# Performance work log

Measured on AMD Instinct MI355X. Metric: run time of the kernel, lower is better.

Reference implementation:

```python
import jax, jax.numpy as jnp
import numpy as np

SLOPE = 25.0  # fast_sigmoid surrogate slope
T, B, N_IN, H, A = 128, 4096, 64, 32, 4
ACT_OUT = 100 * A

@jax.custom_vjp
def spike(x):
    return (x > 0).astype(x.dtype)

def _spk_fwd(x):
    return (x > 0).astype(x.dtype), x

def _spk_bwd(x, g):
    # fast_sigmoid surrogate: d/dx = 1 / (slope*|x| + 1)^2
    return (g / (SLOPE * jnp.abs(x) + 1.0) ** 2,)

spike.defvjp(_spk_fwd, _spk_bwd)

def lif(cur, mem, beta, thr):
    # snntorch Leaky, reset_mechanism='subtract': reset uses previous-step membrane
    reset = spike(mem - thr)
    mem = beta * mem + cur - reset * thr
    return spike(mem - thr), mem

def _linear_init(key, out_d, in_d):
    kw, kb = jax.random.split(key)
    lim = 1.0 / np.sqrt(in_d)
    W = jax.random.uniform(kw, (out_d, in_d), jnp.float32, -lim, lim)
    b = jax.random.uniform(kb, (out_d,), jnp.float32, -lim, lim)
    return W, b

def setup_inputs() -> dict:
    key = jax.random.key(0)
    ks = jax.random.split(key, 12)
    inputs = jax.random.normal(ks[0], (T, B, N_IN), jnp.float32)
    W_in, b_in = _linear_init(ks[1], N_IN, N_IN)
    W1, b1 = _linear_init(ks[2], H, N_IN)
    W2, b2 = _linear_init(ks[3], H, H)
    W3, b3 = _linear_init(ks[4], H, H)
    W4, b4 = _linear_init(ks[5], H, H)
    W5, b5 = _linear_init(ks[6], H, H)
    W6, b6 = _linear_init(ks[7], H, H)
    W7, b7 = _linear_init(ks[8], H, H)
    W_actor, b_actor = _linear_init(ks[9], ACT_OUT, H)
    W_critic, b_critic = _linear_init(ks[10], 1, H)
    beta_critic = jnp.float32(0.95)  # learn_beta=True
    am = np.zeros((ACT_OUT, A), np.float32)
    for row in range(A):
        am[row * 100:(row + 1) * 100, row] = 0.01
    action_mat = jnp.asarray(am)
    return dict(inputs=inputs, W_in=W_in, b_in=b_in, W1=W1, b1=b1, W2=W2, b2=b2,
                W3=W3, b3=b3, W4=W4, b4=b4, W5=W5, b5=b5, W6=W6, b6=b6,
                W7=W7, b7=b7, W_actor=W_actor, b_actor=b_actor,
                W_critic=W_critic, b_critic=b_critic,
                beta_critic=beta_critic, action_mat=action_mat)

def reference(inputs, W_in, b_in, W1, b1, W2, b2, W3, b3, W4, b4, W5, b5,
              W6, b6, W7, b7, W_actor, b_actor, W_critic, b_critic,
              beta_critic, action_mat):
    Bn = inputs.shape[1]
    z = lambda d: jnp.zeros((Bn, d), inputs.dtype)
    carry0 = (z(N_IN), z(H), z(H), z(H), z(H), z(H), z(H), z(H), z(1), z(ACT_OUT))
    layers = ((W1, b1, 0.65, 0.25), (W2, b2, 0.85, 1.0), (W3, b3, 0.85, 1.0),
              (W4, b4, 0.95, 1.0), (W5, b5, 0.95, 1.0), (W6, b6, 0.95, 1.0),
              (W7, b7, 0.95, 1.0))
    def step(carry, x_t):
        m_in, m1, m2, m3, m4, m5, m6, m7, mc, ma = carry
        s, m_in = lif(x_t @ W_in.T + b_in, m_in, 0.65, 0.25)
        mems = [m1, m2, m3, m4, m5, m6, m7]
        new_mems = []
        for (W, b, beta, thr), m in zip(layers, mems):
            s, m = lif(s @ W.T + b, m, beta, thr)
            new_mems.append(m)
        spk_a, ma = lif(s @ W_actor.T + b_actor, ma, 0.95, 1.0)
        _, mc = lif(s @ W_critic.T + b_critic, mc, beta_critic, 100.0)
        val = mc
        actions = spk_a @ action_mat
        return (m_in, *new_mems, mc, ma), (val, actions)
    _, (vals, actions) = jax.lax.scan(step, carry0, inputs)
    return vals, actions  # [T,B,1], [T,B,A]
```

## Files before the change

### kernel.cpp

```cpp
#include <hip/hip_runtime.h>

#define TSTEPS 128
#define BATCH  4096
#define WPB    16

#define OFF_WTIN 0
#define OFF_WT1  4096
#define OFF_WTH  6144
#define OFF_WTA  12288
#define OFF_WC   25088
#define OFF_TAB  25120
#define OFF_XBUF 25224
#define LDS_FLOATS (OFF_XBUF + WPB * 64)
#define LDS_BYTES  (LDS_FLOATS * 4)

#define LIF(M, CUR, BETA, THR) {                                           \
    float r_ = ((M) > (THR)) ? (THR) : 0.0f;                               \
    (M) = __fsub_rn(__fadd_rn(__fmul_rn((BETA), (M)), (CUR)), r_); }

#define HDOT32(MASK, COLP, OUTV) {                                         \
    float acc_ = 0.0f; unsigned mm_ = (MASK);                              \
    while (mm_) {                                                          \
      int j_ = __builtin_ctz(mm_); mm_ &= mm_ - 1;                         \
      acc_ = __fadd_rn(acc_, (COLP)[j_ * 32]);                             \
    }                                                                      \
    OUTV = acc_; }

extern "C" __global__ __launch_bounds__(1024, 1)
void snn_actor_critic(const float* __restrict__ inputs,
                      const float* __restrict__ Win, const float* __restrict__ bin_,
                      const float* __restrict__ W1,  const float* __restrict__ b1,
                      const float* __restrict__ W2,  const float* __restrict__ b2,
                      const float* __restrict__ W3,  const float* __restrict__ b3,
                      const float* __restrict__ W4,  const float* __restrict__ b4,
                      const float* __restrict__ W5,  const float* __restrict__ b5,
                      const float* __restrict__ W6,  const float* __restrict__ b6,
                      const float* __restrict__ W7,  const float* __restrict__ b7,
                      const float* __restrict__ Wa,  const float* __restrict__ ba,
                      const float* __restrict__ Wc,  const float* __restrict__ bc,
                      const float* __restrict__ betac, const float* __restrict__ am,
                      float* __restrict__ out)
{
  extern __shared__ float lds[];
  const int tid  = threadIdx.x;
  const int lane = tid & 63;
  const int l32  = lane & 31;

  #pragma unroll
  for (int it = 0; it < 4; ++it) {
    int idx = tid + it * 1024; int i = idx >> 6, j = idx & 63;
    lds[OFF_WTIN + j * 64 + i] = Win[idx];
  }
  #pragma unroll
  for (int it = 0; it < 2; ++it) {
    int idx = tid + it * 1024; int i = idx >> 6, j = idx & 63;
    lds[OFF_WT1 + j * 32 + i] = W1[idx];
  }
  {
    int i = tid >> 5, j = tid & 31; int d = j * 32 + i;
    lds[OFF_WTH + 0 * 1024 + d] = W2[tid];
    lds[OFF_WTH + 1 * 1024 + d] = W3[tid];
    lds[OFF_WTH + 2 * 1024 + d] = W4[tid];
    lds[OFF_WTH + 3 * 1024 + d] = W5[tid];
    lds[OFF_WTH + 4 * 1024 + d] = W6[tid];
    lds[OFF_WTH + 5 * 1024 + d] = W7[tid];
  }
  for (int idx = tid; idx < 12800; idx += 1024) {
    int k = idx >> 5, j = idx & 31;
    lds[OFF_WTA + j * 400 + k] = Wa[idx];
  }
  if (tid < 32) lds[OFF_WC + tid] = Wc[tid];
  if (tid == 0) {
    float a = 0.0f; lds[OFF_TAB] = 0.0f; float step = am[0];
    for (int n = 1; n <= 100; ++n) { a = __fadd_rn(a, step); lds[OFF_TAB + n] = a; }
  }

  float bin_f = bin_[lane];
  float bh0 = b1[l32], bh1 = b2[l32], bh2 = b3[l32], bh3 = b4[l32],
        bh4 = b5[l32], bh5 = b6[l32], bh6 = b7[l32];
  float ba0 = ba[lane],       ba1 = ba[lane + 64],  ba2 = ba[lane + 128],
        ba3 = ba[lane + 192], ba4 = ba[lane + 256], ba5 = ba[lane + 320],
        ba6 = (lane < 16) ? ba[lane + 384] : 0.0f;
  float bc_f    = bc[0];
  float beta_cf = betac[0];

  __syncthreads();

  const int  wave = tid >> 6;
  const long b    = (long)blockIdx.x * WPB + wave;
  float* xw = lds + OFF_XBUF + wave * 64;
  const float* wcol = lds + OFF_WTIN + lane;
  const float* col1 = lds + OFF_WT1  + l32;
  const float* colh = lds + OFF_WTH  + l32;
  const float* wab  = lds + OFF_WTA  + lane;
  const float* wcp  = lds + OFF_WC;
  const float* tab  = lds + OFF_TAB;
  const float* inp  = inputs + b * 64 + lane;
  float* vout = out + b;
  float* aout = out + (long)TSTEPS * BATCH + b * 4 + lane;

  float m_in = 0.0f;
  float mh0 = 0.0f, mh1 = 0.0f, mh2 = 0.0f, mh3 = 0.0f, mh4 = 0.0f, mh5 = 0.0f, mh6 = 0.0f;
  float ma0 = 0.0f, ma1 = 0.0f, ma2 = 0.0f, ma3 = 0.0f, ma4 = 0.0f, ma5 = 0.0f, ma6 = 0.0f;
  float mc  = 0.0f;

  for (int t = 0; t < TSTEPS; ++t) {
    xw[lane] = inp[(long)t * (BATCH * 64)];

    float acc = 0.0f;
    #pragma unroll
    for (int j = 0; j < 64; ++j)
      acc = __builtin_fmaf(xw[j], wcol[j * 64], acc);
    float cur = __fadd_rn(acc, bin_f);
    LIF(m_in, cur, 0.65f, 0.25f);
    unsigned long long s64 = __ballot(__fsub_rn(m_in, 0.25f) > 0.0f);

    float d1 = 0.0f;
    { unsigned long long mm_ = s64;
      while (mm_) {
        int j_ = (int)__builtin_ctzll(mm_); mm_ &= mm_ - 1;
        d1 = __fadd_rn(d1, col1[j_ * 32]);
      } }
    float cur1 = __fadd_rn(d1, bh0);
    LIF(mh0, cur1, 0.65f, 0.25f);
    unsigned k1 = (unsigned)__ballot(__fsub_rn(mh0, 0.25f) > 0.0f);

    float d2; HDOT32(k1, colh + 0 * 1024, d2);
    float cur2 = __fadd_rn(d2, bh1);
    LIF(mh1, cur2, 0.85f, 1.0f);
    unsigned k2 = (unsigned)__ballot(__fsub_rn(mh1, 1.0f) > 0.0f);

    float d3; HDOT32(k2, colh + 1 * 1024, d3);
    float cur3 = __fadd_rn(d3, bh2);
    LIF(mh2, cur3, 0.85f, 1.0f);
    unsigned k3 = (unsigned)__ballot(__fsub_rn(mh2, 1.0f) > 0.0f);

    float d4; HDOT32(k3, colh + 2 * 1024, d4);
    float cur4 = __fadd_rn(d4, bh3);
    LIF(mh3, cur4, 0.95f, 1.0f);
    unsigned k4 = (unsigned)__ballot(__fsub_rn(mh3, 1.0f) > 0.0f);

    float d5; HDOT32(k4, colh + 3 * 1024, d5);
    float cur5 = __fadd_rn(d5, bh4);
    LIF(mh4, cur5, 0.95f, 1.0f);
    unsigned k5 = (unsigned)__ballot(__fsub_rn(mh4, 1.0f) > 0.0f);

    float d6; HDOT32(k5, colh + 4 * 1024, d6);
    float cur6 = __fadd_rn(d6, bh5);
    LIF(mh5, cur6, 0.95f, 1.0f);
    unsigned k6 = (unsigned)__ballot(__fsub_rn(mh5, 1.0f) > 0.0f);

    float d7; HDOT32(k6, colh + 5 * 1024, d7);
    float cur7 = __fadd_rn(d7, bh6);
    LIF(mh6, cur7, 0.95f, 1.0f);
    unsigned k7 = (unsigned)__ballot(__fsub_rn(mh6, 1.0f) > 0.0f);

    float ca0 = 0.0f, ca1 = 0.0f, ca2 = 0.0f, ca3 = 0.0f, ca4 = 0.0f, ca5 = 0.0f, ca6 = 0.0f;
    { unsigned mm_ = k7;
      while (mm_) {
        int j_ = __builtin_ctz(mm_); mm_ &= mm_ - 1;
        const float* rp = wab + j_ * 400;
        ca0 = __fadd_rn(ca0, rp[0]);   ca1 = __fadd_rn(ca1, rp[64]);
        ca2 = __fadd_rn(ca2, rp[128]); ca3 = __fadd_rn(ca3, rp[192]);
        ca4 = __fadd_rn(ca4, rp[256]); ca5 = __fadd_rn(ca5, rp[320]);
        ca6 = __fadd_rn(ca6, rp[384]);
      } }
    float cua0 = __fadd_rn(ca0, ba0), cua1 = __fadd_rn(ca1, ba1),
          cua2 = __fadd_rn(ca2, ba2), cua3 = __fadd_rn(ca3, ba3),
          cua4 = __fadd_rn(ca4, ba4), cua5 = __fadd_rn(ca5, ba5),
          cua6 = __fadd_rn(ca6, ba6);
    unsigned long long sa0, sa1, sa2, sa3, sa4, sa5, sa6;
    LIF(ma0, cua0, 0.95f, 1.0f); sa0 = __ballot(__fsub_rn(ma0, 1.0f) > 0.0f);
    LIF(ma1, cua1, 0.95f, 1.0f); sa1 = __ballot(__fsub_rn(ma1, 1.0f) > 0.0f);
    LIF(ma2, cua2, 0.95f, 1.0f); sa2 = __ballot(__fsub_rn(ma2, 1.0f) > 0.0f);
    LIF(ma3, cua3, 0.95f, 1.0f); sa3 = __ballot(__fsub_rn(ma3, 1.0f) > 0.0f);
    LIF(ma4, cua4, 0.95f, 1.0f); sa4 = __ballot(__fsub_rn(ma4, 1.0f) > 0.0f);
    LIF(ma5, cua5, 0.95f, 1.0f); sa5 = __ballot(__fsub_rn(ma5, 1.0f) > 0.0f);
    LIF(ma6, cua6, 0.95f, 1.0f); sa6 = __ballot(__fsub_rn(ma6, 1.0f) > 0.0f);

    int c0 = __popcll(sa0) + __popcll(sa1 & 0xFFFFFFFFFULL);
    int c1 = __popcll(sa1 >> 36) + __popcll(sa2) + __popcll(sa3 & 0xFFULL);
    int c2 = __popcll(sa3 >> 8) + __popcll(sa4 & 0xFFFFFFFFFFFULL);
    int c3 = __popcll(sa4 >> 44) + __popcll(sa5) + __popcll(sa6 & 0xFFFFULL);

    float cc = 0.0f;
    { unsigned mm_ = k7;
      while (mm_) { int j_ = __builtin_ctz(mm_); mm_ &= mm_ - 1;
                    cc = __fadd_rn(cc, wcp[j_]); } }
    float curc = __fadd_rn(cc, bc_f);
    LIF(mc, curc, beta_cf, 100.0f);

    if (lane == 0) vout[(long)t * BATCH] = mc;
    if (lane < 4) {
      int cnt = (lane == 0) ? c0 : (lane == 1) ? c1 : (lane == 2) ? c2 : c3;
      aout[(long)t * BATCH * 4] = tab[cnt];
    }
  }
}

extern "C" void kernel_launch(void* const* d_in, const int* in_sizes, int n_in,
                              void* d_out, int out_size, void* d_ws, size_t ws_size,
                              hipStream_t stream) {
  (void)in_sizes; (void)n_in; (void)out_size; (void)d_ws; (void)ws_size;
  hipFuncSetAttribute((const void*)snn_actor_critic,
                      hipFuncAttributeMaxDynamicSharedMemorySize, LDS_BYTES);
  const float* I    = (const float*)d_in[0];
  const float* Win  = (const float*)d_in[1];  const float* bin_ = (const float*)d_in[2];
  const float* W1   = (const float*)d_in[3];  const float* b1   = (const float*)d_in[4];
  const float* W2   = (const float*)d_in[5];  const float* b2   = (const float*)d_in[6];
  const float* W3   = (const float*)d_in[7];  const float* b3   = (const float*)d_in[8];
  const float* W4   = (const float*)d_in[9];  const float* b4   = (const float*)d_in[10];
  const float* W5   = (const float*)d_in[11]; const float* b5   = (const float*)d_in[12];
  const float* W6   = (const float*)d_in[13]; const float* b6   = (const float*)d_in[14];
  const float* W7   = (const float*)d_in[15]; const float* b7   = (const float*)d_in[16];
  const float* Wa   = (const float*)d_in[17]; const float* ba   = (const float*)d_in[18];
  const float* Wc   = (const float*)d_in[19]; const float* bc   = (const float*)d_in[20];
  const float* betc = (const float*)d_in[21]; const float* am   = (const float*)d_in[22];
  float* out = (float*)d_out;

  snn_actor_critic<<<dim3(BATCH / WPB), dim3(1024), LDS_BYTES, stream>>>(
      I, Win, bin_, W1, b1, W2, b2, W3, b3, W4, b4, W5, b5, W6, b6, W7, b7,
      Wa, ba, Wc, bc, betc, am, out);
}
```

Before: 643.7 us.

## Replace sparse spike-mask loops with dense unrolled FMA dot products and prefetch input

Replaces the data-dependent ctz/while loops over spike bitmasks with fully unrolled dense loops that multiply each weight by a 0/1 spike value via FMA. This removes the serial scalar loop control and branch divergence, and lets the LDS loads be issued ahead of time. The cost is doing every multiply-add even when spikes are sparse, which means more LDS traffic. It also software-prefetches the next timestep's input into a register so the global load latency overlaps with the current step's compute.

```diff
diff --git a/kernel.cpp b/kernel.cpp
--- a/kernel.cpp
+++ b/kernel.cpp
@@ -18,11 +18,12 @@
     float r_ = ((M) > (THR)) ? (THR) : 0.0f;                               \
     (M) = __fsub_rn(__fadd_rn(__fmul_rn((BETA), (M)), (CUR)), r_); }
 
-#define HDOT32(MASK, COLP, OUTV) {                                         \
-    float acc_ = 0.0f; unsigned mm_ = (MASK);                              \
-    while (mm_) {                                                          \
-      int j_ = __builtin_ctz(mm_); mm_ &= mm_ - 1;                         \
-      acc_ = __fadd_rn(acc_, (COLP)[j_ * 32]);                             \
+#define DDOT32(MASK, COLP, OUTV) {                                         \
+    float acc_ = 0.0f;                                                     \
+    _Pragma("unroll")                                                      \
+    for (int j_ = 0; j_ < 32; ++j_) {                                      \
+      float sj_ = (((MASK) >> j_) & 1u) ? 1.0f : 0.0f;                     \
+      acc_ = __builtin_fmaf(sj_, (COLP)[j_ * 32], acc_);                   \
     }                                                                      \
     OUTV = acc_; }
 
@@ -104,8 +105,12 @@
   float ma0 = 0.0f, ma1 = 0.0f, ma2 = 0.0f, ma3 = 0.0f, ma4 = 0.0f, ma5 = 0.0f, ma6 = 0.0f;
   float mc  = 0.0f;
 
+  float xnext = inp[0];
+
   for (int t = 0; t < TSTEPS; ++t) {
-    xw[lane] = inp[(long)t * (BATCH * 64)];
+    xw[lane] = xnext;
+    if (t + 1 < TSTEPS)
+      xnext = inp[(long)(t + 1) * (BATCH * 64)];
 
     float acc = 0.0f;
     #pragma unroll
@@ -116,55 +121,58 @@
     unsigned long long s64 = __ballot(__fsub_rn(m_in, 0.25f) > 0.0f);
 
     float d1 = 0.0f;
-    { unsigned long long mm_ = s64;
-      while (mm_) {
-        int j_ = (int)__builtin_ctzll(mm_); mm_ &= mm_ - 1;
-        d1 = __fadd_rn(d1, col1[j_ * 32]);
-      } }
+    #pragma unroll
+    for (int j = 0; j < 64; ++j) {
+      float sj = ((s64 >> j) & 1ULL) ? 1.0f : 0.0f;
+      d1 = __builtin_fmaf(sj, col1[j * 32], d1);
+    }
     float cur1 = __fadd_rn(d1, bh0);
     LIF(mh0, cur1, 0.65f, 0.25f);
     unsigned k1 = (unsigned)__ballot(__fsub_rn(mh0, 0.25f) > 0.0f);
 
-    float d2; HDOT32(k1, colh + 0 * 1024, d2);
+    float d2; DDOT32(k1, colh + 0 * 1024, d2);
     float cur2 = __fadd_rn(d2, bh1);
     LIF(mh1, cur2, 0.85f, 1.0f);
     unsigned k2 = (unsigned)__ballot(__fsub_rn(mh1, 1.0f) > 0.0f);
 
-    float d3; HDOT32(k2, colh + 1 * 1024, d3);
+    float d3; DDOT32(k2, colh + 1 * 1024, d3);
     float cur3 = __fadd_rn(d3, bh2);
     LIF(mh2, cur3, 0.85f, 1.0f);
     unsigned k3 = (unsigned)__ballot(__fsub_rn(mh2, 1.0f) > 0.0f);
 
-    float d4; HDOT32(k3, colh + 2 * 1024, d4);
+    float d4; DDOT32(k3, colh + 2 * 1024, d4);
     float cur4 = __fadd_rn(d4, bh3);
     LIF(mh3, cur4, 0.95f, 1.0f);
     unsigned k4 = (unsigned)__ballot(__fsub_rn(mh3, 1.0f) > 0.0f);
 
-    float d5; HDOT32(k4, colh + 3 * 1024, d5);
+    float d5; DDOT32(k4, colh + 3 * 1024, d5);
     float cur5 = __fadd_rn(d5, bh4);
     LIF(mh4, cur5, 0.95f, 1.0f);
     unsigned k5 = (unsigned)__ballot(__fsub_rn(mh4, 1.0f) > 0.0f);
 
-    float d6; HDOT32(k5, colh + 4 * 1024, d6);
+    float d6; DDOT32(k5, colh + 4 * 1024, d6);
     float cur6 = __fadd_rn(d6, bh5);
     LIF(mh5, cur6, 0.95f, 1.0f);
     unsigned k6 = (unsigned)__ballot(__fsub_rn(mh5, 1.0f) > 0.0f);
 
-    float d7; HDOT32(k6, colh + 5 * 1024, d7);
+    float d7; DDOT32(k6, colh + 5 * 1024, d7);
     float cur7 = __fadd_rn(d7, bh6);
     LIF(mh6, cur7, 0.95f, 1.0f);
     unsigned k7 = (unsigned)__ballot(__fsub_rn(mh6, 1.0f) > 0.0f);
 
     float ca0 = 0.0f, ca1 = 0.0f, ca2 = 0.0f, ca3 = 0.0f, ca4 = 0.0f, ca5 = 0.0f, ca6 = 0.0f;
-    { unsigned mm_ = k7;
-      while (mm_) {
-        int j_ = __builtin_ctz(mm_); mm_ &= mm_ - 1;
-        const float* rp = wab + j_ * 400;
-        ca0 = __fadd_rn(ca0, rp[0]);   ca1 = __fadd_rn(ca1, rp[64]);
-        ca2 = __fadd_rn(ca2, rp[128]); ca3 = __fadd_rn(ca3, rp[192]);
-        ca4 = __fadd_rn(ca4, rp[256]); ca5 = __fadd_rn(ca5, rp[320]);
-        ca6 = __fadd_rn(ca6, rp[384]);
-      } }
+    #pragma unroll
+    for (int j = 0; j < 32; ++j) {
+      float sj = ((k7 >> j) & 1u) ? 1.0f : 0.0f;
+      const float* rp = wab + j * 400;
+      ca0 = __builtin_fmaf(sj, rp[0],   ca0);
+      ca1 = __builtin_fmaf(sj, rp[64],  ca1);
+      ca2 = __builtin_fmaf(sj, rp[128], ca2);
+      ca3 = __builtin_fmaf(sj, rp[192], ca3);
+      ca4 = __builtin_fmaf(sj, rp[256], ca4);
+      ca5 = __builtin_fmaf(sj, rp[320], ca5);
+      ca6 = __builtin_fmaf(sj, rp[384], ca6);
+    }
     float cua0 = __fadd_rn(ca0, ba0), cua1 = __fadd_rn(ca1, ba1),
           cua2 = __fadd_rn(ca2, ba2), cua3 = __fadd_rn(ca3, ba3),
           cua4 = __fadd_rn(ca4, ba4), cua5 = __fadd_rn(ca5, ba5),
@@ -184,9 +192,11 @@
     int c3 = __popcll(sa4 >> 44) + __popcll(sa5) + __popcll(sa6 & 0xFFFFULL);
 
     float cc = 0.0f;
-    { unsigned mm_ = k7;
-      while (mm_) { int j_ = __builtin_ctz(mm_); mm_ &= mm_ - 1;
-                    cc = __fadd_rn(cc, wcp[j_]); } }
+    #pragma unroll
+    for (int j = 0; j < 32; ++j) {
+      float sj = ((k7 >> j) & 1u) ? 1.0f : 0.0f;
+      cc = __builtin_fmaf(sj, wcp[j], cc);
+    }
     float curc = __fadd_rn(cc, bc_f);
     LIF(mc, curc, beta_cf, 100.0f);
 
```

Result: slower. 1.537 ms (+138.8%).

## Process two batch elements per wave with packed FP32 FMAs and dense spike matmuls

Applied to the files above, without the earlier changes.

Each wave now handles two batch elements at once, keeping paired membrane states in float2 and using v_pk_fma_f32 inline asm to evaluate both samples per instruction. The sparse ctz-loop accumulation over spike masks is replaced by fully unrolled dense FMAs, where SGPR-held 0/1 selector pairs multiply interleaved weight pairs. Weights are relaid into float2-interleaved LDS, blocks shrink to 8 waves, and the next timestep's input is prefetched. This removes divergent scalar loops and halves per-sample instruction overhead, but dense FMA changes summation order relative to the sparse adds, which may shift spike thresholds, and it does work even when spikes are sparse.

```diff
diff --git a/kernel.cpp b/kernel.cpp
--- a/kernel.cpp
+++ b/kernel.cpp
@@ -2,31 +2,69 @@
 
 #define TSTEPS 128
 #define BATCH  4096
-#define WPB    16
-
-#define OFF_WTIN 0
-#define OFF_WT1  4096
-#define OFF_WTH  6144
-#define OFF_WTA  12288
-#define OFF_WC   25088
-#define OFF_TAB  25120
-#define OFF_XBUF 25224
-#define LDS_FLOATS (OFF_XBUF + WPB * 64)
+#define WPB    8
+
+typedef float f32x2 __attribute__((ext_vector_type(2)));
+typedef unsigned long long u64;
+
+#define O2_WIN 0
+#define O2_W1  2048
+#define O2_WH  3072
+#define O2_WA  6144
+#define O2_WC  13312
+#define O2_X   13328
+#define TABF   27680
+#define LDS_FLOATS (TABF + 104)
 #define LDS_BYTES  (LDS_FLOATS * 4)
 
-#define LIF(M, CUR, BETA, THR) {                                           \
-    float r_ = ((M) > (THR)) ? (THR) : 0.0f;                               \
-    (M) = __fsub_rn(__fadd_rn(__fmul_rn((BETA), (M)), (CUR)), r_); }
-
-#define HDOT32(MASK, COLP, OUTV) {                                         \
-    float acc_ = 0.0f; unsigned mm_ = (MASK);                              \
-    while (mm_) {                                                          \
-      int j_ = __builtin_ctz(mm_); mm_ &= mm_ - 1;                         \
-      acc_ = __fadd_rn(acc_, (COLP)[j_ * 32]);                             \
-    }                                                                      \
-    OUTV = acc_; }
-
-extern "C" __global__ __launch_bounds__(1024, 1)
+#define C00 0ull
+#define C10 0x3f800000ull
+#define C01 (0x3f800000ull << 32)
+#define C11 (0x3f800000ull | (0x3f800000ull << 32))
+
+#define SEL2(M0, M1, J)                                                    \
+  ((((M0) >> (J)) & 1u) ? ((((M1) >> (J)) & 1u) ? C11 : C10)               \
+                        : ((((M1) >> (J)) & 1u) ? C01 : C00))
+
+#define PKFMA_SLO(ACC, SEL, W2)                                            \
+  asm("v_pk_fma_f32 %0, %1, %2, %0 op_sel:[0,0,0] op_sel_hi:[1,0,1]"       \
+      : "+v"(ACC) : "s"(SEL), "v"(W2))
+#define PKFMA_SHI(ACC, SEL, W2)                                            \
+  asm("v_pk_fma_f32 %0, %1, %2, %0 op_sel:[0,1,0] op_sel_hi:[1,1,1]"       \
+      : "+v"(ACC) : "s"(SEL), "v"(W2))
+#define PKFMA_VLO(ACC, XY, W2)                                             \
+  asm("v_pk_fma_f32 %0, %1, %2, %0 op_sel:[0,0,0] op_sel_hi:[1,0,1]"       \
+      : "+v"(ACC) : "v"(XY), "v"(W2))
+#define PKFMA_VHI(ACC, XY, W2)                                             \
+  asm("v_pk_fma_f32 %0, %1, %2, %0 op_sel:[0,1,0] op_sel_hi:[1,1,1]"       \
+      : "+v"(ACC) : "v"(XY), "v"(W2))
+
+#define LIF2(M, CX, CY, BETA, THR) {                                       \
+    float rx_ = (M[0] > (THR)) ? (THR) : 0.0f;                             \
+    float ry_ = (M[1] > (THR)) ? (THR) : 0.0f;                             \
+    M[0] = __fsub_rn(__fadd_rn(__fmul_rn((BETA), M[0]), (CX)), rx_);       \
+    M[1] = __fsub_rn(__fadd_rn(__fmul_rn((BETA), M[1]), (CY)), ry_); }
+
+#define SPIKES32(M, ACC, BIAS, BETA, THR, M0, M1) {                        \
+    float cx_ = __fadd_rn(ACC[0], (BIAS));                                 \
+    float cy_ = __fadd_rn(ACC[1], (BIAS));                                 \
+    LIF2(M, cx_, cy_, BETA, THR);                                          \
+    u64 b0_ = __ballot(__fsub_rn(M[0], (THR)) > 0.0f);                     \
+    u64 b1_ = __ballot(__fsub_rn(M[1], (THR)) > 0.0f);                     \
+    M0 = __builtin_amdgcn_readfirstlane((unsigned)b0_);                    \
+    M1 = __builtin_amdgcn_readfirstlane((unsigned)b1_); }
+
+#define DENSE32_PK(ACC, BASE2, M0, M1) {                                   \
+    _Pragma("unroll")                                                      \
+    for (int jp_ = 0; jp_ < 16; ++jp_) {                                   \
+      f32x2 w2_ = (BASE2)[jp_ * 32 + i32];                                 \
+      u64 sA_ = SEL2(M0, M1, 2 * jp_);                                     \
+      u64 sB_ = SEL2(M0, M1, 2 * jp_ + 1);                                 \
+      PKFMA_SLO(ACC, sA_, w2_);                                            \
+      PKFMA_SHI(ACC, sB_, w2_);                                            \
+    } }
+
+extern "C" __global__ __launch_bounds__(512, 1)
 void snn_actor_critic(const float* __restrict__ inputs,
                       const float* __restrict__ Win, const float* __restrict__ bin_,
                       const float* __restrict__ W1,  const float* __restrict__ b1,
@@ -42,158 +80,198 @@
                       float* __restrict__ out)
 {
   extern __shared__ float lds[];
+  f32x2* lds2 = (f32x2*)lds;
   const int tid  = threadIdx.x;
   const int lane = tid & 63;
-  const int l32  = lane & 31;
+  const int i32  = lane & 31;
 
   #pragma unroll
   for (int it = 0; it < 4; ++it) {
-    int idx = tid + it * 1024; int i = idx >> 6, j = idx & 63;
-    lds[OFF_WTIN + j * 64 + i] = Win[idx];
+    int e = tid + it * 512; int jp = e >> 6, l = e & 63;
+    lds2[O2_WIN + e] = (f32x2){Win[l * 64 + 2 * jp], Win[l * 64 + 2 * jp + 1]};
   }
   #pragma unroll
   for (int it = 0; it < 2; ++it) {
-    int idx = tid + it * 1024; int i = idx >> 6, j = idx & 63;
-    lds[OFF_WT1 + j * 32 + i] = W1[idx];
+    int e = tid + it * 512; int jp = e >> 5, i = e & 31;
+    lds2[O2_W1 + e] = (f32x2){W1[i * 64 + 2 * jp], W1[i * 64 + 2 * jp + 1]};
   }
   {
-    int i = tid >> 5, j = tid & 31; int d = j * 32 + i;
-    lds[OFF_WTH + 0 * 1024 + d] = W2[tid];
-    lds[OFF_WTH + 1 * 1024 + d] = W3[tid];
-    lds[OFF_WTH + 2 * 1024 + d] = W4[tid];
-    lds[OFF_WTH + 3 * 1024 + d] = W5[tid];
-    lds[OFF_WTH + 4 * 1024 + d] = W6[tid];
-    lds[OFF_WTH + 5 * 1024 + d] = W7[tid];
-  }
-  for (int idx = tid; idx < 12800; idx += 1024) {
-    int k = idx >> 5, j = idx & 31;
-    lds[OFF_WTA + j * 400 + k] = Wa[idx];
-  }
-  if (tid < 32) lds[OFF_WC + tid] = Wc[tid];
+    int jp = tid >> 5, i = tid & 31;
+    lds2[O2_WH + 0 * 512 + tid] = (f32x2){W2[i * 32 + 2 * jp], W2[i * 32 + 2 * jp + 1]};
+    lds2[O2_WH + 1 * 512 + tid] = (f32x2){W3[i * 32 + 2 * jp], W3[i * 32 + 2 * jp + 1]};
+    lds2[O2_WH + 2 * 512 + tid] = (f32x2){W4[i * 32 + 2 * jp], W4[i * 32 + 2 * jp + 1]};
+    lds2[O2_WH + 3 * 512 + tid] = (f32x2){W5[i * 32 + 2 * jp], W5[i * 32 + 2 * jp + 1]};
+    lds2[O2_WH + 4 * 512 + tid] = (f32x2){W6[i * 32 + 2 * jp], W6[i * 32 + 2 * jp + 1]};
+    lds2[O2_WH + 5 * 512 + tid] = (f32x2){W7[i * 32 + 2 * jp], W7[i * 32 + 2 * jp + 1]};
+  }
+  for (int e = tid; e < 7168; e += 512) {
+    int r = e >> 10, rem = e & 1023, jp = rem >> 6, l = rem & 63;
+    int k = r * 64 + l;
+    lds2[O2_WA + e] = (k < 400)
+        ? (f32x2){Wa[k * 32 + 2 * jp], Wa[k * 32 + 2 * jp + 1]}
+        : (f32x2){0.0f, 0.0f};
+  }
+  if (tid < 16) lds2[O2_WC + tid] = (f32x2){Wc[2 * tid], Wc[2 * tid + 1]};
   if (tid == 0) {
-    float a = 0.0f; lds[OFF_TAB] = 0.0f; float step = am[0];
-    for (int n = 1; n <= 100; ++n) { a = __fadd_rn(a, step); lds[OFF_TAB + n] = a; }
+    float a = 0.0f; lds[TABF] = 0.0f; float step = am[0];
+    for (int n = 1; n <= 100; ++n) { a = __fadd_rn(a, step); lds[TABF + n] = a; }
   }
 
   float bin_f = bin_[lane];
-  float bh0 = b1[l32], bh1 = b2[l32], bh2 = b3[l32], bh3 = b4[l32],
-        bh4 = b5[l32], bh5 = b6[l32], bh6 = b7[l32];
-  float ba0 = ba[lane],       ba1 = ba[lane + 64],  ba2 = ba[lane + 128],
-        ba3 = ba[lane + 192], ba4 = ba[lane + 256], ba5 = ba[lane + 320],
-        ba6 = (lane < 16) ? ba[lane + 384] : 0.0f;
-  float bc_f    = bc[0];
+  float bh0 = b1[i32], bh1 = b2[i32], bh2 = b3[i32], bh3 = b4[i32],
+        bh4 = b5[i32], bh5 = b6[i32], bh6 = b7[i32];
+  float bA0 = ba[lane],       bA1 = ba[lane + 64],  bA2 = ba[lane + 128],
+        bA3 = ba[lane + 192], bA4 = ba[lane + 256], bA5 = ba[lane + 320],
+        bA6 = (lane < 16) ? ba[lane + 384] : 0.0f;
+  float bc_f = bc[0];
   float beta_cf = betac[0];
 
   __syncthreads();
 
   const int  wave = tid >> 6;
-  const long b    = (long)blockIdx.x * WPB + wave;
-  float* xw = lds + OFF_XBUF + wave * 64;
-  const float* wcol = lds + OFF_WTIN + lane;
-  const float* col1 = lds + OFF_WT1  + l32;
-  const float* colh = lds + OFF_WTH  + l32;
-  const float* wab  = lds + OFF_WTA  + lane;
-  const float* wcp  = lds + OFF_WC;
-  const float* tab  = lds + OFF_TAB;
-  const float* inp  = inputs + b * 64 + lane;
-  float* vout = out + b;
-  float* aout = out + (long)TSTEPS * BATCH + b * 4 + lane;
-
-  float m_in = 0.0f;
-  float mh0 = 0.0f, mh1 = 0.0f, mh2 = 0.0f, mh3 = 0.0f, mh4 = 0.0f, mh5 = 0.0f, mh6 = 0.0f;
-  float ma0 = 0.0f, ma1 = 0.0f, ma2 = 0.0f, ma3 = 0.0f, ma4 = 0.0f, ma5 = 0.0f, ma6 = 0.0f;
-  float mc  = 0.0f;
+  const long gw   = (long)blockIdx.x * WPB + wave;
+  const long e0   = gw * 2;
+  const f32x2* winb = lds2 + O2_WIN;
+  const f32x2* w1b  = lds2 + O2_W1;
+  const f32x2* whb  = lds2 + O2_WH;
+  const f32x2* wab  = lds2 + O2_WA;
+  const f32x2* wcb  = lds2 + O2_WC;
+  const f32x2* xw2  = lds2 + O2_X + wave * 64;
+  f32x2* xw2w = lds2 + O2_X + wave * 64;
+  const float* tab  = lds + TABF;
+  const float* inp0 = inputs + e0 * 64 + lane;
+  const float* inp1 = inputs + (e0 + 1) * 64 + lane;
+  float* vout = out + e0;
+  float* aout = out + (long)TSTEPS * BATCH + e0 * 4;
+
+  f32x2 mI = {0,0};
+  f32x2 m1 = {0,0}, m2 = {0,0}, m3 = {0,0}, m4 = {0,0}, m5 = {0,0}, m6 = {0,0}, m7 = {0,0};
+  f32x2 A0 = {0,0}, A1 = {0,0}, A2 = {0,0}, A3 = {0,0}, A4 = {0,0}, A5 = {0,0}, A6 = {0,0};
+  f32x2 mc = {0,0};
+
+  float xn0 = inp0[0], xn1 = inp1[0];
 
   for (int t = 0; t < TSTEPS; ++t) {
-    xw[lane] = inp[(long)t * (BATCH * 64)];
-
-    float acc = 0.0f;
+    xw2w[lane] = (f32x2){xn0, xn1};
+    if (t + 1 < TSTEPS) {
+      xn0 = inp0[(long)(t + 1) * (BATCH * 64)];
+      xn1 = inp1[(long)(t + 1) * (BATCH * 64)];
+    }
+
+    f32x2 aI = {0,0};
     #pragma unroll
-    for (int j = 0; j < 64; ++j)
-      acc = __builtin_fmaf(xw[j], wcol[j * 64], acc);
-    float cur = __fadd_rn(acc, bin_f);
-    LIF(m_in, cur, 0.65f, 0.25f);
-    unsigned long long s64 = __ballot(__fsub_rn(m_in, 0.25f) > 0.0f);
-
-    float d1 = 0.0f;
-    { unsigned long long mm_ = s64;
-      while (mm_) {
-        int j_ = (int)__builtin_ctzll(mm_); mm_ &= mm_ - 1;
-        d1 = __fadd_rn(d1, col1[j_ * 32]);
-      } }
-    float cur1 = __fadd_rn(d1, bh0);
-    LIF(mh0, cur1, 0.65f, 0.25f);
-    unsigned k1 = (unsigned)__ballot(__fsub_rn(mh0, 0.25f) > 0.0f);
-
-    float d2; HDOT32(k1, colh + 0 * 1024, d2);
-    float cur2 = __fadd_rn(d2, bh1);
-    LIF(mh1, cur2, 0.85f, 1.0f);
-    unsigned k2 = (unsigned)__ballot(__fsub_rn(mh1, 1.0f) > 0.0f);
-
-    float d3; HDOT32(k2, colh + 1 * 1024, d3);
-    float cur3 = __fadd_rn(d3, bh2);
-    LIF(mh2, cur3, 0.85f, 1.0f);
-    unsigned k3 = (unsigned)__ballot(__fsub_rn(mh2, 1.0f) > 0.0f);
-
-    float d4; HDOT32(k3, colh + 2 * 1024, d4);
-    float cur4 = __fadd_rn(d4, bh3);
-    LIF(mh3, cur4, 0.95f, 1.0f);
-    unsigned k4 = (unsigned)__ballot(__fsub_rn(mh3, 1.0f) > 0.0f);
-
-    float d5; HDOT32(k4, colh + 3 * 1024, d5);
-    float cur5 = __fadd_rn(d5, bh4);
-    LIF(mh4, cur5, 0.95f, 1.0f);
-    unsigned k5 = (unsigned)__ballot(__fsub_rn(mh4, 1.0f) > 0.0f);
-
-    float d6; HDOT32(k5, colh + 4 * 1024, d6);
-    float cur6 = __fadd_rn(d6, bh5);
-    LIF(mh5, cur6, 0.95f, 1.0f);
-    unsigned k6 = (unsigned)__ballot(__fsub_rn(mh5, 1.0f) > 0.0f);
-
-    float d7; HDOT32(k6, colh + 5 * 1024, d7);
-    float cur7 = __fadd_rn(d7, bh6);
-    LIF(mh6, cur7, 0.95f, 1.0f);
-    unsigned k7 = (unsigned)__ballot(__fsub_rn(mh6, 1.0f) > 0.0f);
-
-    float ca0 = 0.0f, ca1 = 0.0f, ca2 = 0.0f, ca3 = 0.0f, ca4 = 0.0f, ca5 = 0.0f, ca6 = 0.0f;
-    { unsigned mm_ = k7;
-      while (mm_) {
-        int j_ = __builtin_ctz(mm_); mm_ &= mm_ - 1;
-        const float* rp = wab + j_ * 400;
-        ca0 = __fadd_rn(ca0, rp[0]);   ca1 = __fadd_rn(ca1, rp[64]);
-        ca2 = __fadd_rn(ca2, rp[128]); ca3 = __fadd_rn(ca3, rp[192]);
-        ca4 = __fadd_rn(ca4, rp[256]); ca5 = __fadd_rn(ca5, rp[320]);
-        ca6 = __fadd_rn(ca6, rp[384]);
-      } }
-    float cua0 = __fadd_rn(ca0, ba0), cua1 = __fadd_rn(ca1, ba1),
-          cua2 = __fadd_rn(ca2, ba2), cua3 = __fadd_rn(ca3, ba3),
-          cua4 = __fadd_rn(ca4, ba4), cua5 = __fadd_rn(ca5, ba5),
-          cua6 = __fadd_rn(ca6, ba6);
-    unsigned long long sa0, sa1, sa2, sa3, sa4, sa5, sa6;
-    LIF(ma0, cua0, 0.95f, 1.0f); sa0 = __ballot(__fsub_rn(ma0, 1.0f) > 0.0f);
-    LIF(ma1, cua1, 0.95f, 1.0f); sa1 = __ballot(__fsub_rn(ma1, 1.0f) > 0.0f);
-    LIF(ma2, cua2, 0.95f, 1.0f); sa2 = __ballot(__fsub_rn(ma2, 1.0f) > 0.0f);
-    LIF(ma3, cua3, 0.95f, 1.0f); sa3 = __ballot(__fsub_rn(ma3, 1.0f) > 0.0f);
-    LIF(ma4, cua4, 0.95f, 1.0f); sa4 = __ballot(__fsub_rn(ma4, 1.0f) > 0.0f);
-    LIF(ma5, cua5, 0.95f, 1.0f); sa5 = __ballot(__fsub_rn(ma5, 1.0f) > 0.0f);
-    LIF(ma6, cua6, 0.95f, 1.0f); sa6 = __ballot(__fsub_rn(ma6, 1.0f) > 0.0f);
-
-    int c0 = __popcll(sa0) + __popcll(sa1 & 0xFFFFFFFFFULL);
-    int c1 = __popcll(sa1 >> 36) + __popcll(sa2) + __popcll(sa3 & 0xFFULL);
-    int c2 = __popcll(sa3 >> 8) + __popcll(sa4 & 0xFFFFFFFFFFFULL);
-    int c3 = __popcll(sa4 >> 44) + __popcll(sa5) + __popcll(sa6 & 0xFFFFULL);
-
-    float cc = 0.0f;
-    { unsigned mm_ = k7;
-      while (mm_) { int j_ = __builtin_ctz(mm_); mm_ &= mm_ - 1;
-                    cc = __fadd_rn(cc, wcp[j_]); } }
-    float curc = __fadd_rn(cc, bc_f);
-    LIF(mc, curc, beta_cf, 100.0f);
-
-    if (lane == 0) vout[(long)t * BATCH] = mc;
-    if (lane < 4) {
-      int cnt = (lane == 0) ? c0 : (lane == 1) ? c1 : (lane == 2) ? c2 : c3;
-      aout[(long)t * BATCH * 4] = tab[cnt];
+    for (int jp = 0; jp < 32; ++jp) {
+      f32x2 w2 = winb[jp * 64 + lane];
+      f32x2 xa = xw2[2 * jp];
+      f32x2 xb = xw2[2 * jp + 1];
+      PKFMA_VLO(aI, xa, w2);
+      PKFMA_VHI(aI, xb, w2);
+    }
+    {
+      float cx = __fadd_rn(aI[0], bin_f), cy = __fadd_rn(aI[1], bin_f);
+      LIF2(mI, cx, cy, 0.65f, 0.25f);
+    }
+    u64 ib0 = __ballot(__fsub_rn(mI[0], 0.25f) > 0.0f);
+    u64 ib1 = __ballot(__fsub_rn(mI[1], 0.25f) > 0.0f);
+    unsigned s0lo = __builtin_amdgcn_readfirstlane((unsigned)ib0);
+    unsigned s0hi = __builtin_amdgcn_readfirstlane((unsigned)(ib0 >> 32));
+    unsigned s1lo = __builtin_amdgcn_readfirstlane((unsigned)ib1);
+    unsigned s1hi = __builtin_amdgcn_readfirstlane((unsigned)(ib1 >> 32));
+
+    f32x2 a1 = {0,0};
+    DENSE32_PK(a1, w1b, s0lo, s1lo);
+    DENSE32_PK(a1, w1b + 16 * 32, s0hi, s1hi);
+    unsigned k1a, k1b; SPIKES32(m1, a1, bh0, 0.65f, 0.25f, k1a, k1b);
+
+    f32x2 a2 = {0,0}; DENSE32_PK(a2, whb + 0 * 512, k1a, k1b);
+    unsigned k2a, k2b; SPIKES32(m2, a2, bh1, 0.85f, 1.0f, k2a, k2b);
+    f32x2 a3 = {0,0}; DENSE32_PK(a3, whb + 1 * 512, k2a, k2b);
+    unsigned k3a, k3b; SPIKES32(m3, a3, bh2, 0.85f, 1.0f, k3a, k3b);
+    f32x2 a4 = {0,0}; DENSE32_PK(a4, whb + 2 * 512, k3a, k3b);
+    unsigned k4a, k4b; SPIKES32(m4, a4, bh3, 0.95f, 1.0f, k4a, k4b);
+    f32x2 a5 = {0,0}; DENSE32_PK(a5, whb + 3 * 512, k4a, k4b);
+    unsigned k5a, k5b; SPIKES32(m5, a5, bh4, 0.95f, 1.0f, k5a, k5b);
+    f32x2 a6 = {0,0}; DENSE32_PK(a6, whb + 4 * 512, k5a, k5b);
+    unsigned k6a, k6b; SPIKES32(m6, a6, bh5, 0.95f, 1.0f, k6a, k6b);
+    f32x2 a7 = {0,0}; DENSE32_PK(a7, whb + 5 * 512, k6a, k6b);
+    unsigned k7a, k7b; SPIKES32(m7, a7, bh6, 0.95f, 1.0f, k7a, k7b);
+
+    f32x2 c0 = {0,0}, c1 = {0,0}, c2 = {0,0}, c3 = {0,0},
+          c4 = {0,0}, c5 = {0,0}, c6 = {0,0}, cc = {0,0};
+    #pragma unroll
+    for (int jp = 0; jp < 16; ++jp) {
+      u64 sA = SEL2(k7a, k7b, 2 * jp);
+      u64 sB = SEL2(k7a, k7b, 2 * jp + 1);
+      f32x2 w0 = wab[0 * 1024 + jp * 64 + lane];
+      f32x2 w1v = wab[1 * 1024 + jp * 64 + lane];
+      f32x2 w2v = wab[2 * 1024 + jp * 64 + lane];
+      f32x2 w3v = wab[3 * 1024 + jp * 64 + lane];
+      f32x2 w4v = wab[4 * 1024 + jp * 64 + lane];
+      f32x2 w5v = wab[5 * 1024 + jp * 64 + lane];
+      f32x2 w6v = wab[6 * 1024 + jp * 64 + lane];
+      f32x2 wcv = wcb[jp];
+      PKFMA_SLO(c0, sA, w0);  PKFMA_SHI(c0, sB, w0);
+      PKFMA_SLO(c1, sA, w1v); PKFMA_SHI(c1, sB, w1v);
+      PKFMA_SLO(c2, sA, w2v); PKFMA_SHI(c2, sB, w2v);
+      PKFMA_SLO(c3, sA, w3v); PKFMA_SHI(c3, sB, w3v);
+      PKFMA_SLO(c4, sA, w4v); PKFMA_SHI(c4, sB, w4v);
+      PKFMA_SLO(c5, sA, w5v); PKFMA_SHI(c5, sB, w5v);
+      PKFMA_SLO(c6, sA, w6v); PKFMA_SHI(c6, sB, w6v);
+      PKFMA_SLO(cc, sA, wcv); PKFMA_SHI(cc, sB, wcv);
+    }
+    u64 sa0, sa1, sa2, sa3, sa4, sa5, sa6;
+    u64 ta0, ta1, ta2, ta3, ta4, ta5, ta6;
+    {
+      float cx, cy;
+      cx = __fadd_rn(c0[0], bA0); cy = __fadd_rn(c0[1], bA0);
+      LIF2(A0, cx, cy, 0.95f, 1.0f);
+      sa0 = __ballot(__fsub_rn(A0[0], 1.0f) > 0.0f);
+      ta0 = __ballot(__fsub_rn(A0[1], 1.0f) > 0.0f);
+      cx = __fadd_rn(c1[0], bA1); cy = __fadd_rn(c1[1], bA1);
+      LIF2(A1, cx, cy, 0.95f, 1.0f);
+      sa1 = __ballot(__fsub_rn(A1[0], 1.0f) > 0.0f);
+      ta1 = __ballot(__fsub_rn(A1[1], 1.0f) > 0.0f);
+      cx = __fadd_rn(c2[0], bA2); cy = __fadd_rn(c2[1], bA2);
+      LIF2(A2, cx, cy, 0.95f, 1.0f);
+      sa2 = __ballot(__fsub_rn(A2[0], 1.0f) > 0.0f);
+      ta2 = __ballot(__fsub_rn(A2[1], 1.0f) > 0.0f);
+      cx = __fadd_rn(c3[0], bA3); cy = __fadd_rn(c3[1], bA3);
+      LIF2(A3, cx, cy, 0.95f, 1.0f);
+      sa3 = __ballot(__fsub_rn(A3[0], 1.0f) > 0.0f);
+      ta3 = __ballot(__fsub_rn(A3[1], 1.0f) > 0.0f);
+      cx = __fadd_rn(c4[0], bA4); cy = __fadd_rn(c4[1], bA4);
+      LIF2(A4, cx, cy, 0.95f, 1.0f);
+      sa4 = __ballot(__fsub_rn(A4[0], 1.0f) > 0.0f);
+      ta4 = __ballot(__fsub_rn(A4[1], 1.0f) > 0.0f);
+      cx = __fadd_rn(c5[0], bA5); cy = __fadd_rn(c5[1], bA5);
+      LIF2(A5, cx, cy, 0.95f, 1.0f);
+      sa5 = __ballot(__fsub_rn(A5[0], 1.0f) > 0.0f);
+      ta5 = __ballot(__fsub_rn(A5[1], 1.0f) > 0.0f);
+      cx = __fadd_rn(c6[0], bA6); cy = __fadd_rn(c6[1], bA6);
+      LIF2(A6, cx, cy, 0.95f, 1.0f);
+      sa6 = __ballot(__fsub_rn(A6[0], 1.0f) > 0.0f);
+      ta6 = __ballot(__fsub_rn(A6[1], 1.0f) > 0.0f);
+    }
+    int g0 = __popcll(sa0) + __popcll(sa1 & 0xFFFFFFFFFULL);
+    int g1 = __popcll(sa1 >> 36) + __popcll(sa2) + __popcll(sa3 & 0xFFULL);
+    int g2 = __popcll(sa3 >> 8) + __popcll(sa4 & 0xFFFFFFFFFFFULL);
+    int g3 = __popcll(sa4 >> 44) + __popcll(sa5) + __popcll(sa6 & 0xFFFFULL);
+    int h0 = __popcll(ta0) + __popcll(ta1 & 0xFFFFFFFFFULL);
+    int h1 = __popcll(ta1 >> 36) + __popcll(ta2) + __popcll(ta3 & 0xFFULL);
+    int h2 = __popcll(ta3 >> 8) + __popcll(ta4 & 0xFFFFFFFFFFFULL);
+    int h3 = __popcll(ta4 >> 44) + __popcll(ta5) + __popcll(ta6 & 0xFFFFULL);
+
+    {
+      float cx = __fadd_rn(cc[0], bc_f), cy = __fadd_rn(cc[1], bc_f);
+      LIF2(mc, cx, cy, beta_cf, 100.0f);
+    }
+
+    if (lane < 2) vout[(long)t * BATCH + lane] = (lane ? mc[1] : mc[0]);
+    if (lane < 8) {
+      int g = lane & 3;
+      int cnt = (lane >= 4) ? (g == 0 ? h0 : g == 1 ? h1 : g == 2 ? h2 : h3)
+                            : (g == 0 ? g0 : g == 1 ? g1 : g == 2 ? g2 : g3);
+      aout[(long)t * (BATCH * 4) + lane] = tab[cnt];
     }
   }
 }
@@ -218,7 +296,7 @@
   const float* betc = (const float*)d_in[21]; const float* am   = (const float*)d_in[22];
   float* out = (float*)d_out;
 
-  snn_actor_critic<<<dim3(BATCH / WPB), dim3(1024), LDS_BYTES, stream>>>(
+  snn_actor_critic<<<dim3(BATCH / (WPB * 2)), dim3(512), LDS_BYTES, stream>>>(
       I, Win, bin_, W1, b1, W2, b2, W3, b3, W4, b4, W5, b5, W6, b6, W7, b7,
       Wa, ba, Wc, bc, betc, am, out);
 }
```

Measured after the change: 1.323 ms. 106% more time.
